# Performance work log

Measured on AMD Instinct MI355X. Metric: run time of the kernel, lower is better.

Reference implementation:

```python
import jax, jax.numpy as jnp
import numpy as np

B, L, D = 1, 512, 1024
NH, NKV, NR = 16, 4, 16
HD, RD = 64, 64
NREP = NH // NKV  # 4
ATTN_SCALE = 1.0 / float(np.sqrt(HD))
REL_SCALE = 1.0 / float(np.sqrt(RD))


def setup_inputs() -> dict:
    key = jax.random.key(0)
    ks = jax.random.split(key, 9)
    x = jax.random.normal(ks[0], (B, L, D), jnp.float32)
    symbols = jax.random.normal(ks[1], (B, L, D), jnp.float32)
    # standard llama-style RoPE frequencies: [L, HD//2]
    inv_freq = 1.0 / (10000.0 ** (np.arange(0, HD, 2, dtype=np.float32) / HD))
    f = np.outer(np.arange(L, dtype=np.float32), inv_freq)
    freqs_cos = jnp.asarray(np.cos(f), jnp.float32)
    freqs_sin = jnp.asarray(np.sin(f), jnp.float32)
    s = 0.02
    wq_attn = jax.random.normal(ks[2], (D, NH * HD), jnp.float32) * s
    wk_attn = jax.random.normal(ks[3], (D, NKV * HD), jnp.float32) * s
    wq_rel = jax.random.normal(ks[4], (D, NR * RD), jnp.float32) * s
    wk_rel = jax.random.normal(ks[5], (D, NR * RD), jnp.float32) * s
    wr = jax.random.normal(ks[6], (NR, NH * HD), jnp.float32) * s
    wv = jax.random.normal(ks[7], (D, NKV * HD), jnp.float32) * s
    wo = jax.random.normal(ks[8], (NH * HD, NH * HD), jnp.float32) * s
    return dict(x=x, symbols=symbols, freqs_cos=freqs_cos, freqs_sin=freqs_sin,
                wq_attn=wq_attn, wk_attn=wk_attn, wq_rel=wq_rel, wk_rel=wk_rel,
                wr=wr, wv=wv, wo=wo)


def _rope(t, cos, sin):
    # t: [b, l, h, hd]; cos/sin: [l, hd//2]
    tr = t.reshape(t.shape[:-1] + (HD // 2, 2))
    re, im = tr[..., 0], tr[..., 1]
    c = cos[None, :, None, :]
    s = sin[None, :, None, :]
    out = jnp.stack([re * c - im * s, re * s + im * c], axis=-1)
    return out.reshape(t.shape)


def reference(x, symbols, freqs_cos, freqs_sin, wq_attn, wk_attn, wq_rel, wk_rel, wr, wv, wo):
    b, l, _ = x.shape
    q = (x @ wq_attn).reshape(b, l, NH, HD)
    k = (x @ wk_attn).reshape(b, l, NKV, HD)
    qr = (x @ wq_rel).reshape(b, l, NR, RD)
    kr = (x @ wk_rel).reshape(b, l, NR, RD)
    sv = (symbols @ wv).reshape(b, l, NKV, HD)
    q = _rope(q, freqs_cos, freqs_sin)
    k = _rope(k, freqs_cos, freqs_sin)
    # GQA: repeat kv heads consecutively (matches torch repeat_kv expand+reshape)
    k = jnp.repeat(k, NREP, axis=2)
    sv = jnp.repeat(sv, NREP, axis=2)
    scores = jnp.einsum('bihd,bjhd->bhij', q, k) * ATTN_SCALE
    causal = jnp.tril(jnp.ones((l, l), bool))
    scores = jnp.where(causal[None, None], scores, -jnp.inf)
    attn = jax.nn.softmax(scores, axis=-1)  # [b, nh, l, l]
    # relation scores, identity activation, laid out as [b, i, j, nr]
    relations = jnp.einsum('bird,bjrd->bijr', qr, kr) * REL_SCALE
    proj_rel = (relations @ wr).reshape(b, l, l, NH, HD)  # dominant intermediate
    attended_symbols = jnp.einsum('bhij,bjhd->bihd', attn, sv)
    attended_relations = jnp.einsum('bhij,bijhd->bihd', attn, proj_rel)
    out = (attended_symbols + attended_relations).reshape(b, l, NH * HD) @ wo
    return out, attn, relations
```

## Files before the change

kernel.cpp:

```cpp
#include <hip/hip_runtime.h>
#include <math.h>

#define ATTN_SCALE 0.125f
#define REL_SCALE 0.125f

using ushort = unsigned short;
using bf16x8 = __attribute__((ext_vector_type(8))) __bf16;
using floatx4 = __attribute__((ext_vector_type(4))) float;
using ushort8 = __attribute__((ext_vector_type(8))) ushort;
using ushort4v = __attribute__((ext_vector_type(4))) ushort;

__device__ __forceinline__ ushort f2bf(float x) {
  unsigned int u = __builtin_bit_cast(unsigned int, x);
  u += 0x7fffu + ((u >> 16) & 1u);
  return (ushort)(u >> 16);
}

__device__ __forceinline__ void mfma_body(const ushort* __restrict__ A, int lda,
                                          const ushort* __restrict__ Bt, int ldb,
                                          int K, floatx4 (&acc)[2][2]) {
  __shared__ ushort As[64][72];
  __shared__ ushort Bs[64][72];
  const int tid = threadIdx.x;
  const int sr = tid >> 2, sc = (tid & 3) << 4;
  const int lane = tid & 63;
  const int wy = (tid >> 7) & 1, wx = (tid >> 6) & 1;
  const int lm = lane & 15, lq = lane >> 4;
  const ushort* a_rd = &As[32 * wy + lm][lq * 8];
  const ushort* b_rd = &Bs[32 * wx + lm][lq * 8];
  for (int k0 = 0; k0 < K; k0 += 64) {
    const ushort* Ap = A + (size_t)sr * lda + k0 + sc;
    ushort8 av0 = *(const ushort8*)Ap;
    ushort8 av1 = *(const ushort8*)(Ap + 8);
    const ushort* Bp = Bt + (size_t)sr * ldb + k0 + sc;
    ushort8 bv0 = *(const ushort8*)Bp;
    ushort8 bv1 = *(const ushort8*)(Bp + 8);
    __syncthreads();
    *(ushort8*)&As[sr][sc] = av0;
    *(ushort8*)&As[sr][sc + 8] = av1;
    *(ushort8*)&Bs[sr][sc] = bv0;
    *(ushort8*)&Bs[sr][sc + 8] = bv1;
    __syncthreads();
#pragma unroll
    for (int kh = 0; kh < 2; ++kh) {
      bf16x8 a0 = *(const bf16x8*)(a_rd + kh * 32);
      bf16x8 a1 = *(const bf16x8*)(a_rd + 16 * 72 + kh * 32);
      bf16x8 b0 = *(const bf16x8*)(b_rd + kh * 32);
      bf16x8 b1 = *(const bf16x8*)(b_rd + 16 * 72 + kh * 32);
      acc[0][0] = __builtin_amdgcn_mfma_f32_16x16x32_bf16(a0, b0, acc[0][0], 0, 0, 0);
      acc[0][1] = __builtin_amdgcn_mfma_f32_16x16x32_bf16(a0, b1, acc[0][1], 0, 0, 0);
      acc[1][0] = __builtin_amdgcn_mfma_f32_16x16x32_bf16(a1, b0, acc[1][0], 0, 0, 0);
      acc[1][1] = __builtin_amdgcn_mfma_f32_16x16x32_bf16(a1, b1, acc[1][1], 0, 0, 0);
    }
  }
}

#define EPILOG_VARS                                                   \
  const int lane = threadIdx.x & 63;                                  \
  const int wy = (threadIdx.x >> 7) & 1, wx = (threadIdx.x >> 6) & 1; \
  const int lm = lane & 15, lq = lane >> 4;

__global__ __launch_bounds__(256) void prep_kernel(
    const float* __restrict__ x, const float* __restrict__ sym,
    const float* __restrict__ wq, const float* __restrict__ wk,
    const float* __restrict__ wqr, const float* __restrict__ wkr,
    const float* __restrict__ wv, const float* __restrict__ wo,
    ushort* __restrict__ xb, ushort* __restrict__ symb,
    ushort* __restrict__ wqT, ushort* __restrict__ wkT, ushort* __restrict__ wqrT,
    ushort* __restrict__ wkrT, ushort* __restrict__ wvT, ushort* __restrict__ woT) {
  if (blockIdx.z == 6) {
    int b = blockIdx.y * 32 + blockIdx.x;
    if (b >= 512) return;
    int idx = b * 256 + threadIdx.x;
    int i4 = idx << 2;
    float4 v = *(const float4*)(x + i4);
    uint2 o;
    o.x = (unsigned)f2bf(v.x) | ((unsigned)f2bf(v.y) << 16);
    o.y = (unsigned)f2bf(v.z) | ((unsigned)f2bf(v.w) << 16);
    *(uint2*)(xb + i4) = o;
    float4 w = *(const float4*)(sym + i4);
    o.x = (unsigned)f2bf(w.x) | ((unsigned)f2bf(w.y) << 16);
    o.y = (unsigned)f2bf(w.z) | ((unsigned)f2bf(w.w) << 16);
    *(uint2*)(symb + i4) = o;
    return;
  }
  __shared__ ushort t[32][33];
  const float* in;
  ushort* out;
  int N;
  switch (blockIdx.z) {
    case 0: in = wq;  out = wqT;  N = 1024; break;
    case 1: in = wk;  out = wkT;  N = 256;  break;
    case 2: in = wqr; out = wqrT; N = 1024; break;
    case 3: in = wkr; out = wkrT; N = 1024; break;
    case 4: in = wv;  out = wvT;  N = 256;  break;
    default: in = wo; out = woT;  N = 1024; break;
  }
  int n0 = blockIdx.x << 5;
  if (n0 >= N) return;
  int k0 = blockIdx.y << 5;
  int tx = threadIdx.x & 31, ty = threadIdx.x >> 5;
#pragma unroll
  for (int rr = 0; rr < 32; rr += 8)
    t[ty + rr][tx] = f2bf(in[(size_t)(k0 + ty + rr) * N + n0 + tx]);
  __syncthreads();
#pragma unroll
  for (int rr = 0; rr < 32; rr += 8)
    out[(size_t)(n0 + ty + rr) * 1024 + k0 + tx] = t[tx][ty + rr];
}

__global__ __launch_bounds__(256) void proj_mfma(
    const ushort* __restrict__ xb, const ushort* __restrict__ symb,
    const ushort* __restrict__ wqT, const ushort* __restrict__ wkT,
    const ushort* __restrict__ wqrT, const ushort* __restrict__ wkrT,
    const ushort* __restrict__ wvT,
    ushort* __restrict__ qb, ushort* __restrict__ kb, ushort* __restrict__ qrb,
    ushort* __restrict__ krb, ushort* __restrict__ svT,
    const float* __restrict__ fcos, const float* __restrict__ fsin) {
  const int z = blockIdx.z;
  const ushort* A = xb;
  const ushort* Bt;
  ushort* C;
  int N;
  switch (z) {
    case 0: Bt = wqT;  C = qb;  N = 1024; break;
    case 1: Bt = wkT;  C = kb;  N = 256;  break;
    case 2: Bt = wqrT; C = qrb; N = 1024; break;
    case 3: Bt = wkrT; C = krb; N = 1024; break;
    default: A = symb; Bt = wvT; C = svT; N = 256; break;
  }
  const int bn = blockIdx.x << 6;
  if (bn >= N) return;
  const int bm = blockIdx.y << 6;
  floatx4 acc[2][2] = {};
  mfma_body(A + (size_t)bm * 1024, 1024, Bt + (size_t)bn * 1024, 1024, 1024, acc);
  EPILOG_VARS
  if (z <= 1) {
#pragma unroll
    for (int sy = 0; sy < 2; ++sy)
#pragma unroll
      for (int sx = 0; sx < 2; ++sx)
#pragma unroll
        for (int e = 0; e < 4; ++e) {
          int row = bm + 32 * wy + 16 * sy + 4 * lq + e;
          int col = bn + 32 * wx + 16 * sx + lm;
          float v = acc[sy][sx][e];
          float pv = __shfl_xor(v, 1);
          int d = col & 63, p = d >> 1;
          float c = fcos[(row << 5) + p], s = fsin[(row << 5) + p];
          float o = (d & 1) ? fmaf(pv, s, v * c) : fmaf(v, c, -pv * s);
          C[(size_t)row * N + col] = f2bf(o);
        }
  } else if (z == 4) {
#pragma unroll
    for (int sy = 0; sy < 2; ++sy)
#pragma unroll
      for (int sx = 0; sx < 2; ++sx)
#pragma unroll
        for (int e = 0; e < 4; ++e) {
          int row = bm + 32 * wy + 16 * sy + 4 * lq + e;
          int col = bn + 32 * wx + 16 * sx + lm;
          svT[(size_t)col * 512 + row] = f2bf(acc[sy][sx][e]);
        }
  } else {
#pragma unroll
    for (int sy = 0; sy < 2; ++sy)
#pragma unroll
      for (int sx = 0; sx < 2; ++sx)
#pragma unroll
        for (int e = 0; e < 4; ++e) {
          int row = bm + 32 * wy + 16 * sy + 4 * lq + e;
          int col = bn + 32 * wx + 16 * sx + lm;
          C[(size_t)row * N + col] = f2bf(acc[sy][sx][e]);
        }
  }
}

__global__ __launch_bounds__(256) void relflash_kernel(
    const ushort* __restrict__ qb, const ushort* __restrict__ kb,
    const ushort* __restrict__ svT, const ushort* __restrict__ qrb,
    const ushort* __restrict__ krb, float* __restrict__ attn,
    float* __restrict__ asym, float* __restrict__ rel,
    ushort* __restrict__ rel_bT) {
  __shared__ float S[16][516];
  __shared__ ushort P[16][520];
  const int bx = blockIdx.x;
  const int tid = threadIdx.x, wave = tid >> 6, lane = tid & 63;
  const int lm = lane & 15, lq = lane >> 4;
  if (bx >= 512) {
    const int b = bx - 512;
    const int bi0 = (b >> 4) << 5, bj0 = (b & 15) << 5;
    const int ib = bi0 + ((wave >> 1) << 4), jb = bj0 + ((wave & 1) << 4);
    const ushort* qrow = qrb + (size_t)(ib + lm) * 1024 + lq * 8;
    const ushort* krow = krb + (size_t)(jb + lm) * 1024 + lq * 8;
#pragma unroll
    for (int rq = 0; rq < 4; ++rq) {
      floatx4 acc[4];
#pragma unroll
      for (int rr = 0; rr < 4; ++rr) {
        int roff = ((rq << 2) + rr) << 6;
        bf16x8 a0 = *(const bf16x8*)(qrow + roff);
        bf16x8 a1 = *(const bf16x8*)(qrow + roff + 32);
        bf16x8 b0 = *(const bf16x8*)(krow + roff);
        bf16x8 b1 = *(const bf16x8*)(krow + roff + 32);
        floatx4 t = {0.f, 0.f, 0.f, 0.f};
        t = __builtin_amdgcn_mfma_f32_16x16x32_bf16(a0, b0, t, 0, 0, 0);
        t = __builtin_amdgcn_mfma_f32_16x16x32_bf16(a1, b1, t, 0, 0, 0);
        acc[rr] = t;
      }
#pragma unroll
      for (int e = 0; e < 4; ++e) {
        int i = ib + 4 * lq + e, j = jb + lm;
        float4 v = make_float4(acc[0][e] * REL_SCALE, acc[1][e] * REL_SCALE,
                               acc[2][e] * REL_SCALE, acc[3][e] * REL_SCALE);
        *(float4*)(rel + ((size_t)i * 512 + j) * 16 + (rq << 2)) = v;
        size_t tb = (size_t)i * 8192 + (size_t)(rq << 2) * 512 + j;
        rel_bT[tb]         = f2bf(v.x);
        rel_bT[tb + 512]   = f2bf(v.y);
        rel_bT[tb + 1024]  = f2bf(v.z);
        rel_bT[tb + 1536]  = f2bf(v.w);
      }
    }
    return;
  }
  const int h = bx >> 5, it = 31 - (bx & 31);
  const int i0 = it << 4, kv = h >> 2;
  const int ntiles = it + 1;
  const ushort* qrow = qb + (size_t)(i0 + lm) * 1024 + (h << 6) + lq * 8;
  bf16x8 a0 = *(const bf16x8*)(qrow);
  bf16x8 a1 = *(const bf16x8*)(qrow + 32);
  for (int jt = wave; jt < ntiles; jt += 4) {
    int jb = jt << 4;
    const ushort* krow = kb + (size_t)(jb + lm) * 256 + (kv << 6) + lq * 8;
    bf16x8 b0 = *(const bf16x8*)(krow);
    bf16x8 b1 = *(const bf16x8*)(krow + 32);
    floatx4 acc = {0.f, 0.f, 0.f, 0.f};
    acc = __builtin_amdgcn_mfma_f32_16x16x32_bf16(a0, b0, acc, 0, 0, 0);
    acc = __builtin_amdgcn_mfma_f32_16x16x32_bf16(a1, b1, acc, 0, 0, 0);
#pragma unroll
    for (int e = 0; e < 4; ++e) S[4 * lq + e][jb + lm] = acc[e] * ATTN_SCALE;
  }
  __syncthreads();
  const int row = tid >> 4, t16 = tid & 15;
  const int i = i0 + row;
  const int nj = ntiles << 4;
  float m = -INFINITY;
  for (int s = 0; (s << 6) < nj; ++s) {
    int j4 = (t16 << 2) + (s << 6);
    float4 v = *(const float4*)&S[row][j4];
    if (j4 + 0 <= i) m = fmaxf(m, v.x);
    if (j4 + 1 <= i) m = fmaxf(m, v.y);
    if (j4 + 2 <= i) m = fmaxf(m, v.z);
    if (j4 + 3 <= i) m = fmaxf(m, v.w);
  }
#pragma unroll
  for (int o = 8; o; o >>= 1) m = fmaxf(m, __shfl_xor(m, o, 16));
  float sum = 0.f;
  for (int s = 0; (s << 6) < nj; ++s) {
    int j4 = (t16 << 2) + (s << 6);
    float4 v = *(const float4*)&S[row][j4];
    v.x = (j4 + 0 <= i) ? __expf(v.x - m) : 0.f;
    v.y = (j4 + 1 <= i) ? __expf(v.y - m) : 0.f;
    v.z = (j4 + 2 <= i) ? __expf(v.z - m) : 0.f;
    v.w = (j4 + 3 <= i) ? __expf(v.w - m) : 0.f;
    sum += v.x + v.y + v.z + v.w;
    *(float4*)&S[row][j4] = v;
  }
#pragma unroll
  for (int o = 8; o; o >>= 1) sum += __shfl_xor(sum, o, 16);
  const float inv = 1.f / sum;
  float* arow = attn + (size_t)h * 262144 + (size_t)i * 512;
  for (int s = 0; s < 8; ++s) {
    int j4 = (t16 << 2) + (s << 6);
    float4 o4 = {0.f, 0.f, 0.f, 0.f};
    if (j4 < nj) {
      float4 v = *(const float4*)&S[row][j4];
      o4.x = v.x * inv;
      o4.y = v.y * inv;
      o4.z = v.z * inv;
      o4.w = v.w * inv;
    }
    *(float4*)(arow + j4) = o4;
    ushort4v p4;
    p4.x = f2bf(o4.x); p4.y = f2bf(o4.y); p4.z = f2bf(o4.z); p4.w = f2bf(o4.w);
    *(ushort4v*)&P[row][j4] = p4;
  }
  __syncthreads();
  const int dbase = wave << 4;
  floatx4 acc2 = {0.f, 0.f, 0.f, 0.f};
  const ushort* svrow = svT + (size_t)((kv << 6) + dbase + lm) * 512;
  const int kmax = (nj + 31) & ~31;
  for (int kt = 0; kt < kmax; kt += 32) {
    bf16x8 pa = *(const bf16x8*)&P[lm][kt + lq * 8];
    bf16x8 pb = *(const bf16x8*)(svrow + kt + lq * 8);
    acc2 = __builtin_amdgcn_mfma_f32_16x16x32_bf16(pa, pb, acc2, 0, 0, 0);
  }
#pragma unroll
  for (int e = 0; e < 4; ++e)
    asym[(size_t)(i0 + 4 * lq + e) * 1024 + (h << 6) + dbase + lm] = acc2[e];
}

__global__ __launch_bounds__(256) void tker_combine(const float* __restrict__ attn,
                                                    const ushort* __restrict__ rel_bT,
                                                    const float* __restrict__ asym,
                                                    const float* __restrict__ wr,
                                                    ushort* __restrict__ attb) {
  const int i0 = blockIdx.x << 2;
  const int tid = threadIdx.x, wave = tid >> 6, lane = tid & 63;
  const int lm = lane & 15, lq = lane >> 4;
  const int i = i0 + wave;
  __shared__ float Ts[4][16][17];
  floatx4 acc = {0.f, 0.f, 0.f, 0.f};
  const float* arow = attn + (size_t)lm * 262144 + (size_t)i * 512;
  const ushort* brow = rel_bT + (size_t)i * 8192 + (size_t)lm * 512;
  const int ktiles = (i >> 5) + 1;
  for (int kt = 0; kt < ktiles; ++kt) {
    int k = (kt << 5) + lq * 8;
    float4 f0 = *(const float4*)(arow + k);
    float4 f1 = *(const float4*)(arow + k + 4);
    bf16x8 a = __builtin_bit_cast(bf16x8,
        ushort8{f2bf(f0.x), f2bf(f0.y), f2bf(f0.z), f2bf(f0.w),
                f2bf(f1.x), f2bf(f1.y), f2bf(f1.z), f2bf(f1.w)});
    bf16x8 b = *(const bf16x8*)(brow + k);
    acc = __builtin_amdgcn_mfma_f32_16x16x32_bf16(a, b, acc, 0, 0, 0);
  }
#pragma unroll
  for (int e = 0; e < 4; ++e) Ts[wave][4 * lq + e][lm] = acc[e];
  __syncthreads();
  const int hc = tid >> 4, d4 = (tid & 15) << 2;
  float4 o[4];
#pragma unroll
  for (int iw = 0; iw < 4; ++iw)
    o[iw] = *(const float4*)(asym + (size_t)(i0 + iw) * 1024 + (hc << 6) + d4);
#pragma unroll
  for (int rr = 0; rr < 16; ++rr) {
    float4 w4 = *(const float4*)(wr + (size_t)rr * 1024 + (hc << 6) + d4);
#pragma unroll
    for (int iw = 0; iw < 4; ++iw) {
      float tv = Ts[iw][hc][rr];
      o[iw].x = fmaf(tv, w4.x, o[iw].x);
      o[iw].y = fmaf(tv, w4.y, o[iw].y);
      o[iw].z = fmaf(tv, w4.z, o[iw].z);
      o[iw].w = fmaf(tv, w4.w, o[iw].w);
    }
  }
#pragma unroll
  for (int iw = 0; iw < 4; ++iw) {
    ushort4v ob;
    ob.x = f2bf(o[iw].x); ob.y = f2bf(o[iw].y);
    ob.z = f2bf(o[iw].z); ob.w = f2bf(o[iw].w);
    *(ushort4v*)(attb + (size_t)(i0 + iw) * 1024 + (hc << 6) + d4) = ob;
  }
}

__global__ __launch_bounds__(256) void out_mfma(const ushort* __restrict__ attb,
                                                const ushort* __restrict__ woT,
                                                float* __restrict__ out) {
  __shared__ ushort As[64][72];
  __shared__ ushort Bs[32][72];
  const int bn = blockIdx.x << 5, bm = blockIdx.y << 6;
  const int tid = threadIdx.x;
  const int sr = tid >> 2, sc = (tid & 3) << 4;
  const int br = tid >> 3, bc = (tid & 7) << 3;
  const int lane = tid & 63;
  const int wy = (tid >> 7) & 1, wx = (tid >> 6) & 1;
  const int lm = lane & 15, lq = lane >> 4;
  const ushort* a_rd = &As[32 * wy + lm][lq * 8];
  const ushort* b_rd = &Bs[16 * wx + lm][lq * 8];
  floatx4 acc[2] = {};
  for (int k0 = 0; k0 < 1024; k0 += 64) {
    const ushort* Ap = attb + (size_t)(bm + sr) * 1024 + k0 + sc;
    ushort8 av0 = *(const ushort8*)Ap;
    ushort8 av1 = *(const ushort8*)(Ap + 8);
    ushort8 bv = *(const ushort8*)(woT + (size_t)(bn + br) * 1024 + k0 + bc);
    __syncthreads();
    *(ushort8*)&As[sr][sc] = av0;
    *(ushort8*)&As[sr][sc + 8] = av1;
    *(ushort8*)&Bs[br][bc] = bv;
    __syncthreads();
#pragma unroll
    for (int kh = 0; kh < 2; ++kh) {
      bf16x8 a0 = *(const bf16x8*)(a_rd + kh * 32);
      bf16x8 a1 = *(const bf16x8*)(a_rd + 16 * 72 + kh * 32);
      bf16x8 b0 = *(const bf16x8*)(b_rd + kh * 32);
      acc[0] = __builtin_amdgcn_mfma_f32_16x16x32_bf16(a0, b0, acc[0], 0, 0, 0);
      acc[1] = __builtin_amdgcn_mfma_f32_16x16x32_bf16(a1, b0, acc[1], 0, 0, 0);
    }
  }
#pragma unroll
  for (int sy = 0; sy < 2; ++sy)
#pragma unroll
    for (int e = 0; e < 4; ++e) {
      int row = bm + 32 * wy + 16 * sy + 4 * lq + e;
      int col = bn + 16 * wx + lm;
      out[(size_t)row * 1024 + col] = acc[sy][e];
    }
}

extern "C" void kernel_launch(void* const* d_in, const int* in_sizes, int n_in,
                              void* d_out, int out_size, void* d_ws, size_t ws_size,
                              hipStream_t stream) {
  const float* x       = (const float*)d_in[0];
  const float* symbols = (const float*)d_in[1];
  const float* fcos    = (const float*)d_in[2];
  const float* fsin    = (const float*)d_in[3];
  const float* wq_attn = (const float*)d_in[4];
  const float* wk_attn = (const float*)d_in[5];
  const float* wq_rel  = (const float*)d_in[6];
  const float* wk_rel  = (const float*)d_in[7];
  const float* wr      = (const float*)d_in[8];
  const float* wv      = (const float*)d_in[9];
  const float* wo      = (const float*)d_in[10];

  float* out  = (float*)d_out;
  float* attn = out + 524288;
  float* rel  = attn + 4194304;

  char* wsb = (char*)d_ws;
  const size_t KB = 1024;
  ushort* xb     = (ushort*)(wsb);
  ushort* symb   = (ushort*)(wsb + 1024 * KB);
  ushort* wqT    = (ushort*)(wsb + 2048 * KB);
  ushort* wkT    = (ushort*)(wsb + 4096 * KB);
  ushort* wqrT   = (ushort*)(wsb + 4608 * KB);
  ushort* wkrT   = (ushort*)(wsb + 6656 * KB);
  ushort* wvT    = (ushort*)(wsb + 8704 * KB);
  ushort* woT    = (ushort*)(wsb + 9216 * KB);
  ushort* qb     = (ushort*)(wsb + 11264 * KB);
  ushort* kb     = (ushort*)(wsb + 12288 * KB);
  ushort* qrb    = (ushort*)(wsb + 12544 * KB);
  ushort* krb    = (ushort*)(wsb + 13568 * KB);
  ushort* svT    = (ushort*)(wsb + 14592 * KB);
  float*  asym   = (float*)(wsb + 14848 * KB);
  ushort* attb   = (ushort*)(wsb + 16896 * KB);
  ushort* rel_bT = (ushort*)(wsb + 17920 * KB);

  prep_kernel<<<dim3(32, 32, 7), 256, 0, stream>>>(x, symbols, wq_attn, wk_attn,
                                                   wq_rel, wk_rel, wv, wo,
                                                   xb, symb, wqT, wkT, wqrT, wkrT, wvT, woT);
  proj_mfma<<<dim3(16, 8, 5), 256, 0, stream>>>(xb, symb, wqT, wkT, wqrT, wkrT, wvT,
                                                qb, kb, qrb, krb, svT, fcos, fsin);
  relflash_kernel<<<dim3(768), 256, 0, stream>>>(qb, kb, svT, qrb, krb, attn, asym,
                                                 rel, rel_bT);
  tker_combine<<<dim3(128), 256, 0, stream>>>(attn, rel_bT, asym, wr, attb);
  out_mfma<<<dim3(32, 8), 256, 0, stream>>>(attb, woT, out);
}
```

Before: 152.9 us.

## Halve projection GEMM N-tile and stash bf16 attention in i-major layout

The projection GEMM now uses 64x32 output tiles instead of 64x64, doubling the grid so more workgroups are available across the CUs. The attention kernel also writes a bf16 copy of the probabilities in an i-major [i][h][j] layout. The combine kernel reads that copy directly instead of gathering fp32 attention rows strided across heads and converting them. This trades an extra bf16 write in the attention kernel for half-size, contiguous reads in the combine step, and costs less A-tile reuse per projection block.

```diff
diff --git a/kernel.cpp b/kernel.cpp
--- a/kernel.cpp
+++ b/kernel.cpp
@@ -15,50 +15,6 @@
   u += 0x7fffu + ((u >> 16) & 1u);
   return (ushort)(u >> 16);
 }
-
-__device__ __forceinline__ void mfma_body(const ushort* __restrict__ A, int lda,
-                                          const ushort* __restrict__ Bt, int ldb,
-                                          int K, floatx4 (&acc)[2][2]) {
-  __shared__ ushort As[64][72];
-  __shared__ ushort Bs[64][72];
-  const int tid = threadIdx.x;
-  const int sr = tid >> 2, sc = (tid & 3) << 4;
-  const int lane = tid & 63;
-  const int wy = (tid >> 7) & 1, wx = (tid >> 6) & 1;
-  const int lm = lane & 15, lq = lane >> 4;
-  const ushort* a_rd = &As[32 * wy + lm][lq * 8];
-  const ushort* b_rd = &Bs[32 * wx + lm][lq * 8];
-  for (int k0 = 0; k0 < K; k0 += 64) {
-    const ushort* Ap = A + (size_t)sr * lda + k0 + sc;
-    ushort8 av0 = *(const ushort8*)Ap;
-    ushort8 av1 = *(const ushort8*)(Ap + 8);
-    const ushort* Bp = Bt + (size_t)sr * ldb + k0 + sc;
-    ushort8 bv0 = *(const ushort8*)Bp;
-    ushort8 bv1 = *(const ushort8*)(Bp + 8);
-    __syncthreads();
-    *(ushort8*)&As[sr][sc] = av0;
-    *(ushort8*)&As[sr][sc + 8] = av1;
-    *(ushort8*)&Bs[sr][sc] = bv0;
-    *(ushort8*)&Bs[sr][sc + 8] = bv1;
-    __syncthreads();
-#pragma unroll
-    for (int kh = 0; kh < 2; ++kh) {
-      bf16x8 a0 = *(const bf16x8*)(a_rd + kh * 32);
-      bf16x8 a1 = *(const bf16x8*)(a_rd + 16 * 72 + kh * 32);
-      bf16x8 b0 = *(const bf16x8*)(b_rd + kh * 32);
-      bf16x8 b1 = *(const bf16x8*)(b_rd + 16 * 72 + kh * 32);
-      acc[0][0] = __builtin_amdgcn_mfma_f32_16x16x32_bf16(a0, b0, acc[0][0], 0, 0, 0);
-      acc[0][1] = __builtin_amdgcn_mfma_f32_16x16x32_bf16(a0, b1, acc[0][1], 0, 0, 0);
-      acc[1][0] = __builtin_amdgcn_mfma_f32_16x16x32_bf16(a1, b0, acc[1][0], 0, 0, 0);
-      acc[1][1] = __builtin_amdgcn_mfma_f32_16x16x32_bf16(a1, b1, acc[1][1], 0, 0, 0);
-    }
-  }
-}
-
-#define EPILOG_VARS                                                   \
-  const int lane = threadIdx.x & 63;                                  \
-  const int wy = (threadIdx.x >> 7) & 1, wx = (threadIdx.x >> 6) & 1; \
-  const int lm = lane & 15, lq = lane >> 4;
 
 __global__ __launch_bounds__(256) void prep_kernel(
     const float* __restrict__ x, const float* __restrict__ sym,
@@ -117,6 +73,8 @@
     ushort* __restrict__ qb, ushort* __restrict__ kb, ushort* __restrict__ qrb,
     ushort* __restrict__ krb, ushort* __restrict__ svT,
     const float* __restrict__ fcos, const float* __restrict__ fsin) {
+  __shared__ ushort As[64][72];
+  __shared__ ushort Bs[32][72];
   const int z = blockIdx.z;
   const ushort* A = xb;
   const ushort* Bt;
@@ -129,50 +87,69 @@
     case 3: Bt = wkrT; C = krb; N = 1024; break;
     default: A = symb; Bt = wvT; C = svT; N = 256; break;
   }
-  const int bn = blockIdx.x << 6;
+  const int bn = blockIdx.x << 5;
   if (bn >= N) return;
   const int bm = blockIdx.y << 6;
-  floatx4 acc[2][2] = {};
-  mfma_body(A + (size_t)bm * 1024, 1024, Bt + (size_t)bn * 1024, 1024, 1024, acc);
-  EPILOG_VARS
+  const int tid = threadIdx.x;
+  const int sr = tid >> 2, sc = (tid & 3) << 4;
+  const int br = tid >> 3, bc = (tid & 7) << 3;
+  const int lane = tid & 63;
+  const int wy = (tid >> 7) & 1, wx = (tid >> 6) & 1;
+  const int lm = lane & 15, lq = lane >> 4;
+  const ushort* a_rd = &As[32 * wy + lm][lq * 8];
+  const ushort* b_rd = &Bs[16 * wx + lm][lq * 8];
+  floatx4 acc[2] = {};
+  for (int k0 = 0; k0 < 1024; k0 += 64) {
+    const ushort* Ap = A + (size_t)(bm + sr) * 1024 + k0 + sc;
+    ushort8 av0 = *(const ushort8*)Ap;
+    ushort8 av1 = *(const ushort8*)(Ap + 8);
+    ushort8 bv = *(const ushort8*)(Bt + (size_t)(bn + br) * 1024 + k0 + bc);
+    __syncthreads();
+    *(ushort8*)&As[sr][sc] = av0;
+    *(ushort8*)&As[sr][sc + 8] = av1;
+    *(ushort8*)&Bs[br][bc] = bv;
+    __syncthreads();
+#pragma unroll
+    for (int kh = 0; kh < 2; ++kh) {
+      bf16x8 a0 = *(const bf16x8*)(a_rd + kh * 32);
+      bf16x8 a1 = *(const bf16x8*)(a_rd + 16 * 72 + kh * 32);
+      bf16x8 b0 = *(const bf16x8*)(b_rd + kh * 32);
+      acc[0] = __builtin_amdgcn_mfma_f32_16x16x32_bf16(a0, b0, acc[0], 0, 0, 0);
+      acc[1] = __builtin_amdgcn_mfma_f32_16x16x32_bf16(a1, b0, acc[1], 0, 0, 0);
+    }
+  }
   if (z <= 1) {
 #pragma unroll
     for (int sy = 0; sy < 2; ++sy)
 #pragma unroll
-      for (int sx = 0; sx < 2; ++sx)
-#pragma unroll
-        for (int e = 0; e < 4; ++e) {
-          int row = bm + 32 * wy + 16 * sy + 4 * lq + e;
-          int col = bn + 32 * wx + 16 * sx + lm;
-          float v = acc[sy][sx][e];
-          float pv = __shfl_xor(v, 1);
-          int d = col & 63, p = d >> 1;
-          float c = fcos[(row << 5) + p], s = fsin[(row << 5) + p];
-          float o = (d & 1) ? fmaf(pv, s, v * c) : fmaf(v, c, -pv * s);
-          C[(size_t)row * N + col] = f2bf(o);
-        }
+      for (int e = 0; e < 4; ++e) {
+        int row = bm + 32 * wy + 16 * sy + 4 * lq + e;
+        int col = bn + 16 * wx + lm;
+        float v = acc[sy][e];
+        float pv = __shfl_xor(v, 1);
+        int d = col & 63, p = d >> 1;
+        float c = fcos[(row << 5) + p], s = fsin[(row << 5) + p];
+        float o = (d & 1) ? fmaf(pv, s, v * c) : fmaf(v, c, -pv * s);
+        C[(size_t)row * N + col] = f2bf(o);
+      }
   } else if (z == 4) {
 #pragma unroll
     for (int sy = 0; sy < 2; ++sy)
 #pragma unroll
-      for (int sx = 0; sx < 2; ++sx)
-#pragma unroll
-        for (int e = 0; e < 4; ++e) {
-          int row = bm + 32 * wy + 16 * sy + 4 * lq + e;
-          int col = bn + 32 * wx + 16 * sx + lm;
-          svT[(size_t)col * 512 + row] = f2bf(acc[sy][sx][e]);
-        }
+      for (int e = 0; e < 4; ++e) {
+        int row = bm + 32 * wy + 16 * sy + 4 * lq + e;
+        int col = bn + 16 * wx + lm;
+        svT[(size_t)col * 512 + row] = f2bf(acc[sy][e]);
+      }
   } else {
 #pragma unroll
     for (int sy = 0; sy < 2; ++sy)
 #pragma unroll
-      for (int sx = 0; sx < 2; ++sx)
-#pragma unroll
-        for (int e = 0; e < 4; ++e) {
-          int row = bm + 32 * wy + 16 * sy + 4 * lq + e;
-          int col = bn + 32 * wx + 16 * sx + lm;
-          C[(size_t)row * N + col] = f2bf(acc[sy][sx][e]);
-        }
+      for (int e = 0; e < 4; ++e) {
+        int row = bm + 32 * wy + 16 * sy + 4 * lq + e;
+        int col = bn + 16 * wx + lm;
+        C[(size_t)row * N + col] = f2bf(acc[sy][e]);
+      }
   }
 }
 
@@ -180,8 +157,8 @@
     const ushort* __restrict__ qb, const ushort* __restrict__ kb,
     const ushort* __restrict__ svT, const ushort* __restrict__ qrb,
     const ushort* __restrict__ krb, float* __restrict__ attn,
-    float* __restrict__ asym, float* __restrict__ rel,
-    ushort* __restrict__ rel_bT) {
+    ushort* __restrict__ attn_b, float* __restrict__ asym,
+    float* __restrict__ rel, ushort* __restrict__ rel_bT) {
   __shared__ float S[16][516];
   __shared__ ushort P[16][520];
   const int bx = blockIdx.x;
@@ -215,10 +192,10 @@
                                acc[2][e] * REL_SCALE, acc[3][e] * REL_SCALE);
         *(float4*)(rel + ((size_t)i * 512 + j) * 16 + (rq << 2)) = v;
         size_t tb = (size_t)i * 8192 + (size_t)(rq << 2) * 512 + j;
-        rel_bT[tb]         = f2bf(v.x);
-        rel_bT[tb + 512]   = f2bf(v.y);
-        rel_bT[tb + 1024]  = f2bf(v.z);
-        rel_bT[tb + 1536]  = f2bf(v.w);
+        rel_bT[tb]        = f2bf(v.x);
+        rel_bT[tb + 512]  = f2bf(v.y);
+        rel_bT[tb + 1024] = f2bf(v.z);
+        rel_bT[tb + 1536] = f2bf(v.w);
       }
     }
     return;
@@ -270,6 +247,7 @@
   for (int o = 8; o; o >>= 1) sum += __shfl_xor(sum, o, 16);
   const float inv = 1.f / sum;
   float* arow = attn + (size_t)h * 262144 + (size_t)i * 512;
+  ushort* abrow = attn_b + (size_t)i * 8192 + (size_t)h * 512;
   for (int s = 0; s < 8; ++s) {
     int j4 = (t16 << 2) + (s << 6);
     float4 o4 = {0.f, 0.f, 0.f, 0.f};
@@ -284,6 +262,7 @@
     ushort4v p4;
     p4.x = f2bf(o4.x); p4.y = f2bf(o4.y); p4.z = f2bf(o4.z); p4.w = f2bf(o4.w);
     *(ushort4v*)&P[row][j4] = p4;
+    *(ushort4v*)(abrow + j4) = p4;
   }
   __syncthreads();
   const int dbase = wave << 4;
@@ -300,7 +279,7 @@
     asym[(size_t)(i0 + 4 * lq + e) * 1024 + (h << 6) + dbase + lm] = acc2[e];
 }
 
-__global__ __launch_bounds__(256) void tker_combine(const float* __restrict__ attn,
+__global__ __launch_bounds__(256) void tker_combine(const ushort* __restrict__ attn_b,
                                                     const ushort* __restrict__ rel_bT,
                                                     const float* __restrict__ asym,
                                                     const float* __restrict__ wr,
@@ -311,16 +290,12 @@
   const int i = i0 + wave;
   __shared__ float Ts[4][16][17];
   floatx4 acc = {0.f, 0.f, 0.f, 0.f};
-  const float* arow = attn + (size_t)lm * 262144 + (size_t)i * 512;
+  const ushort* arow = attn_b + (size_t)i * 8192 + (size_t)lm * 512;
   const ushort* brow = rel_bT + (size_t)i * 8192 + (size_t)lm * 512;
   const int ktiles = (i >> 5) + 1;
   for (int kt = 0; kt < ktiles; ++kt) {
     int k = (kt << 5) + lq * 8;
-    float4 f0 = *(const float4*)(arow + k);
-    float4 f1 = *(const float4*)(arow + k + 4);
-    bf16x8 a = __builtin_bit_cast(bf16x8,
-        ushort8{f2bf(f0.x), f2bf(f0.y), f2bf(f0.z), f2bf(f0.w),
-                f2bf(f1.x), f2bf(f1.y), f2bf(f1.z), f2bf(f1.w)});
+    bf16x8 a = *(const bf16x8*)(arow + k);
     bf16x8 b = *(const bf16x8*)(brow + k);
     acc = __builtin_amdgcn_mfma_f32_16x16x32_bf16(a, b, acc, 0, 0, 0);
   }
@@ -434,14 +409,15 @@
   float*  asym   = (float*)(wsb + 14848 * KB);
   ushort* attb   = (ushort*)(wsb + 16896 * KB);
   ushort* rel_bT = (ushort*)(wsb + 17920 * KB);
+  ushort* attn_b = (ushort*)(wsb + 26112 * KB);
 
   prep_kernel<<<dim3(32, 32, 7), 256, 0, stream>>>(x, symbols, wq_attn, wk_attn,
                                                    wq_rel, wk_rel, wv, wo,
                                                    xb, symb, wqT, wkT, wqrT, wkrT, wvT, woT);
-  proj_mfma<<<dim3(16, 8, 5), 256, 0, stream>>>(xb, symb, wqT, wkT, wqrT, wkrT, wvT,
+  proj_mfma<<<dim3(32, 8, 5), 256, 0, stream>>>(xb, symb, wqT, wkT, wqrT, wkrT, wvT,
                                                 qb, kb, qrb, krb, svT, fcos, fsin);
-  relflash_kernel<<<dim3(768), 256, 0, stream>>>(qb, kb, svT, qrb, krb, attn, asym,
-                                                 rel, rel_bT);
-  tker_combine<<<dim3(128), 256, 0, stream>>>(attn, rel_bT, asym, wr, attb);
+  relflash_kernel<<<dim3(768), 256, 0, stream>>>(qb, kb, svT, qrb, krb, attn, attn_b,
+                                                 asym, rel, rel_bT);
+  tker_combine<<<dim3(128), 256, 0, stream>>>(attn_b, rel_bT, asym, wr, attb);
   out_mfma<<<dim3(32, 8), 256, 0, stream>>>(attb, woT, out);
 }
```

Result: no change. 153.1 us, median of 2 (+0.1%).
